# Kernel tuning notes

Hardware: AMD Instinct MI355X
Metric: run time of the kernel (lower is better)

Reference implementation:

```python
import jax, jax.numpy as jnp
import numpy as np

BATCH, L, E = 8192, 4096, 12  # E = log2(L) butterfly stages


def setup_inputs() -> dict:
    key = jax.random.key(0)
    kx, kw = jax.random.split(key)
    x = jax.random.normal(kx, (BATCH, L), dtype=jnp.float32)
    # Stacked per-stage weights: stage s has an (L, 2) coefficient table
    # (matches nn.Parameter(torch.randn(L, 2)) for each of E stages).
    W = jax.random.normal(kw, (E, L, 2), dtype=jnp.float32)
    return {"x": x, "W": W}


def _butterfly(x, W):
    # rightmost=True: apply the smallest-stride factor first (stride 1 -> L/2).
    B = x.shape[0]
    e = W.shape[0]
    y = x
    for s in range(e):
        d = 1 << s                      # pairing stride at this stage
        g = L // (2 * d)                # number of butterfly groups
        yr = y.reshape(B, g, 2, d)      # pairs (i, i ^ d) along last dim
        Wr = W[s].reshape(g, 2, d, 2)   # per-row 2x2 mix coefficients
        top, bot = yr[:, :, 0, :], yr[:, :, 1, :]
        new_top = Wr[:, 0, :, 0] * top + Wr[:, 0, :, 1] * bot
        new_bot = Wr[:, 1, :, 0] * bot + Wr[:, 1, :, 1] * top
        y = jnp.stack([new_top, new_bot], axis=2).reshape(B, L)
    return y


def reference(x, W):
    return _butterfly(x, W)
```

## Files before the change

### kernel.cpp

```cpp
#include <hip/hip_runtime.h>


constexpr int LROW = 4096;
constexpr int RPB  = 4;
constexpr int NBLK = 8192 / RPB;

__device__ __forceinline__ int sig(int p) { return p ^ ((p >> 5) & 31); }

__global__ __launch_bounds__(256, 2)
void butterfly12_kernel(const float* __restrict__ x,
                        const float* __restrict__ W,
                        float* __restrict__ out)
{
    __shared__ float lds[RPB * LROW];

    const int t    = threadIdx.x;
    const int hi   = t >> 4;
    const int lo   = t & 15;
    const int row0 = blockIdx.x * RPB;

    float v[RPB][16];

    #pragma unroll
    for (int r = 0; r < RPB; ++r) {
        const float4* xr = reinterpret_cast<const float4*>(x + (size_t)(row0 + r) * LROW);
        #pragma unroll
        for (int m = 0; m < 4; ++m) {
            const float4 q = xr[t * 4 + m];
            v[r][4*m+0] = q.x; v[r][4*m+1] = q.y;
            v[r][4*m+2] = q.z; v[r][4*m+3] = q.w;
        }
    }

    #pragma unroll
    for (int b = 0; b < 4; ++b) {
        const int s = b;
        float2 ws[16];
        const float4* wq = reinterpret_cast<const float4*>(W + ((size_t)s * LROW + t * 16) * 2);
        #pragma unroll
        for (int m = 0; m < 8; ++m) {
            const float4 q = wq[m];
            ws[2*m]   = make_float2(q.x, q.y);
            ws[2*m+1] = make_float2(q.z, q.w);
        }
        const int dl = 1 << b;
        #pragma unroll
        for (int g = 0; g < 16; g += 2*dl)
            #pragma unroll
            for (int m = 0; m < dl; ++m) {
                const int a = g + m, c = a + dl;
                #pragma unroll
                for (int r = 0; r < RPB; ++r) {
                    const float va = v[r][a], vb = v[r][c];
                    v[r][a] = ws[a].x * va + ws[a].y * vb;
                    v[r][c] = ws[c].x * vb + ws[c].y * va;
                }
            }
    }

    #pragma unroll
    for (int r = 0; r < RPB; ++r)
        #pragma unroll
        for (int i = 0; i < 16; ++i)
            lds[r * LROW + sig(16*t + i)] = v[r][i];
    __syncthreads();
    #pragma unroll
    for (int r = 0; r < RPB; ++r)
        #pragma unroll
        for (int j = 0; j < 16; ++j)
            v[r][j] = lds[r * LROW + sig(hi*256 + j*16 + lo)];

    #pragma unroll
    for (int b = 0; b < 4; ++b) {
        const int s = 4 + b;
        float2 ws[16];
        #pragma unroll
        for (int j = 0; j < 16; ++j)
            ws[j] = *reinterpret_cast<const float2*>(W + ((size_t)s * LROW + hi*256 + j*16 + lo) * 2);
        const int dl = 1 << b;
        #pragma unroll
        for (int g = 0; g < 16; g += 2*dl)
            #pragma unroll
            for (int m = 0; m < dl; ++m) {
                const int a = g + m, c = a + dl;
                #pragma unroll
                for (int r = 0; r < RPB; ++r) {
                    const float va = v[r][a], vb = v[r][c];
                    v[r][a] = ws[a].x * va + ws[a].y * vb;
                    v[r][c] = ws[c].x * vb + ws[c].y * va;
                }
            }
    }

    #pragma unroll
    for (int r = 0; r < RPB; ++r)
        #pragma unroll
        for (int j = 0; j < 16; ++j)
            lds[r * LROW + sig(hi*256 + j*16 + lo)] = v[r][j];
    __syncthreads();
    #pragma unroll
    for (int r = 0; r < RPB; ++r)
        #pragma unroll
        for (int k = 0; k < 16; ++k)
            v[r][k] = lds[r * LROW + sig(k*256 + t)];

    #pragma unroll
    for (int b = 0; b < 4; ++b) {
        const int s = 8 + b;
        float2 ws[16];
        #pragma unroll
        for (int k = 0; k < 16; ++k)
            ws[k] = *reinterpret_cast<const float2*>(W + ((size_t)s * LROW + k*256 + t) * 2);
        const int dl = 1 << b;
        #pragma unroll
        for (int g = 0; g < 16; g += 2*dl)
            #pragma unroll
            for (int m = 0; m < dl; ++m) {
                const int a = g + m, c = a + dl;
                #pragma unroll
                for (int r = 0; r < RPB; ++r) {
                    const float va = v[r][a], vb = v[r][c];
                    v[r][a] = ws[a].x * va + ws[a].y * vb;
                    v[r][c] = ws[c].x * vb + ws[c].y * va;
                }
            }
    }

    #pragma unroll
    for (int r = 0; r < RPB; ++r) {
        float* orow = out + (size_t)(row0 + r) * LROW;
        #pragma unroll
        for (int k = 0; k < 16; ++k)
            orow[k*256 + t] = v[r][k];
    }
}

extern "C" void kernel_launch(void* const* d_in, const int* in_sizes, int n_in,
                              void* d_out, int out_size, void* d_ws, size_t ws_size,
                              hipStream_t stream) {
    const float* x = (const float*)d_in[0];
    const float* W = (const float*)d_in[1];
    float* out = (float*)d_out;

    butterfly12_kernel<<<NBLK, 256, 0, stream>>>(x, W, out);
}
```

Baseline: 277.3 us.

## Halve LDS staging to raise occupancy and use nontemporal global accesses

The LDS transpose buffer shrinks from four rows to two, and each transpose runs in two passes with extra barriers. Launch bounds are raised so more blocks can be resident per CU. Input loads and output stores become nontemporal to avoid polluting the cache with streaming data. The tighter register budget risks spilling the 64-value per-thread state, and the extra barriers add sync cost.

```diff
diff --git a/kernel.cpp b/kernel.cpp
--- a/kernel.cpp
+++ b/kernel.cpp
@@ -5,14 +5,16 @@
 constexpr int RPB  = 4;
 constexpr int NBLK = 8192 / RPB;
 
+typedef float f32x4 __attribute__((ext_vector_type(4)));
+
 __device__ __forceinline__ int sig(int p) { return p ^ ((p >> 5) & 31); }
 
-__global__ __launch_bounds__(256, 2)
+__global__ __launch_bounds__(256, 5)
 void butterfly12_kernel(const float* __restrict__ x,
                         const float* __restrict__ W,
                         float* __restrict__ out)
 {
-    __shared__ float lds[RPB * LROW];
+    __shared__ float lds[2 * LROW];
 
     const int t    = threadIdx.x;
     const int hi   = t >> 4;
@@ -23,10 +25,10 @@
 
     #pragma unroll
     for (int r = 0; r < RPB; ++r) {
-        const float4* xr = reinterpret_cast<const float4*>(x + (size_t)(row0 + r) * LROW);
+        const f32x4* xr = reinterpret_cast<const f32x4*>(x + (size_t)(row0 + r) * LROW);
         #pragma unroll
         for (int m = 0; m < 4; ++m) {
-            const float4 q = xr[t * 4 + m];
+            const f32x4 q = __builtin_nontemporal_load(&xr[t * 4 + m]);
             v[r][4*m+0] = q.x; v[r][4*m+1] = q.y;
             v[r][4*m+2] = q.z; v[r][4*m+3] = q.w;
         }
@@ -59,16 +61,20 @@
     }
 
     #pragma unroll
-    for (int r = 0; r < RPB; ++r)
+    for (int rr = 0; rr < RPB; rr += 2) {
         #pragma unroll
-        for (int i = 0; i < 16; ++i)
-            lds[r * LROW + sig(16*t + i)] = v[r][i];
-    __syncthreads();
-    #pragma unroll
-    for (int r = 0; r < RPB; ++r)
+        for (int r = 0; r < 2; ++r)
+            #pragma unroll
+            for (int i = 0; i < 16; ++i)
+                lds[r * LROW + sig(16*t + i)] = v[rr + r][i];
+        __syncthreads();
         #pragma unroll
-        for (int j = 0; j < 16; ++j)
-            v[r][j] = lds[r * LROW + sig(hi*256 + j*16 + lo)];
+        for (int r = 0; r < 2; ++r)
+            #pragma unroll
+            for (int j = 0; j < 16; ++j)
+                v[rr + r][j] = lds[r * LROW + sig(hi*256 + j*16 + lo)];
+        if (rr + 2 < RPB) __syncthreads();
+    }
 
     #pragma unroll
     for (int b = 0; b < 4; ++b) {
@@ -93,16 +99,20 @@
     }
 
     #pragma unroll
-    for (int r = 0; r < RPB; ++r)
+    for (int rr = 0; rr < RPB; rr += 2) {
         #pragma unroll
-        for (int j = 0; j < 16; ++j)
-            lds[r * LROW + sig(hi*256 + j*16 + lo)] = v[r][j];
-    __syncthreads();
-    #pragma unroll
-    for (int r = 0; r < RPB; ++r)
+        for (int r = 0; r < 2; ++r)
+            #pragma unroll
+            for (int j = 0; j < 16; ++j)
+                lds[r * LROW + sig(hi*256 + j*16 + lo)] = v[rr + r][j];
+        __syncthreads();
         #pragma unroll
-        for (int k = 0; k < 16; ++k)
-            v[r][k] = lds[r * LROW + sig(k*256 + t)];
+        for (int r = 0; r < 2; ++r)
+            #pragma unroll
+            for (int k = 0; k < 16; ++k)
+                v[rr + r][k] = lds[r * LROW + sig(k*256 + t)];
+        if (rr + 2 < RPB) __syncthreads();
+    }
 
     #pragma unroll
     for (int b = 0; b < 4; ++b) {
@@ -131,7 +141,7 @@
         float* orow = out + (size_t)(row0 + r) * LROW;
         #pragma unroll
         for (int k = 0; k < 16; ++k)
-            orow[k*256 + t] = v[r][k];
+            __builtin_nontemporal_store(v[r][k], &orow[k*256 + t]);
     }
 }
 
```

New measurement: 336.2 us. 21.3% more time.
